# Kernel tuning notes

Hardware: AMD Instinct MI355X
Metric: run time of the kernel (lower is better)

Reference implementation:

```python
import jax, jax.numpy as jnp
import numpy as np

N_CELL = 66
N_SUB = 29934
N = N_CELL + N_SUB  # 30000 nodes
F = 256
E_HALF = 480000
K = 3
LAYERS = 2
BN_EPS = 1e-5


def setup_inputs() -> dict:
    key = jax.random.key(0)
    ks = jax.random.split(key, 8)
    cell_feat = jax.random.normal(ks[0], (N_CELL, F), dtype=jnp.float32)
    sub_feat = jax.random.normal(ks[1], (N_SUB, F), dtype=jnp.float32)
    # interaction_edge builds a symmetric directed edge list: (a,b) and (b,a)
    src = jax.random.randint(ks[2], (E_HALF,), 0, N)
    dst = jax.random.randint(ks[3], (E_HALF,), 0, N)
    edge_index = jnp.stack([jnp.concatenate([src, dst]),
                            jnp.concatenate([dst, src])], axis=0)
    ew_half = jax.random.uniform(ks[4], (E_HALF,), dtype=jnp.float32, minval=0.1, maxval=1.0)
    edge_weight = jnp.concatenate([ew_half, ew_half])
    glorot = np.sqrt(6.0 / (F + F))
    W1 = jax.random.uniform(ks[5], (F, F), dtype=jnp.float32, minval=-glorot, maxval=glorot)
    W2 = jax.random.uniform(ks[6], (F, F), dtype=jnp.float32, minval=-glorot, maxval=glorot)
    b1 = jnp.zeros((F,), jnp.float32)
    b2 = jnp.zeros((F,), jnp.float32)
    prelu_w = jnp.full((F,), 0.25, jnp.float32)  # PReLU default init
    gamma = jnp.ones((F,), jnp.float32)
    beta = jnp.zeros((F,), jnp.float32)
    return {"cell_feat": cell_feat, "sub_feat": sub_feat,
            "edge_index": edge_index, "edge_weight": edge_weight,
            "W1": W1, "b1": b1, "W2": W2, "b2": b2,
            "prelu_w": prelu_w, "gamma": gamma, "beta": beta}


def _gcn_norm(edge_index, edge_weight, n):
    # SGConv's gcn_norm: add self-loops (weight 1), symmetric degree normalization
    loop = jnp.arange(n)
    row = jnp.concatenate([edge_index[0], loop])  # source j
    col = jnp.concatenate([edge_index[1], loop])  # target i
    ew = jnp.concatenate([edge_weight, jnp.ones((n,), edge_weight.dtype)])
    deg = jax.ops.segment_sum(ew, col, num_segments=n)
    dinv = jnp.where(deg > 0, jax.lax.rsqrt(deg), 0.0)
    norm = dinv[row] * ew * dinv[col]
    return row, col, norm


def _sgconv(x, row, col, norm, W, b, n):
    # K-hop propagation: x <- A_hat^K x, then linear
    for _ in range(K):
        x = jax.ops.segment_sum(norm[:, None] * x[row], col, num_segments=n)
    return x @ W.T + b


def _prelu_bn(x, prelu_w, gamma, beta):
    x = jnp.where(x >= 0, x, prelu_w * x)
    mean = jnp.mean(x, axis=0)
    var = jnp.mean(jnp.square(x - mean), axis=0)  # biased, training-mode BN
    return gamma * (x - mean) * jax.lax.rsqrt(var + BN_EPS) + beta


def reference(cell_feat, sub_feat, edge_index, edge_weight,
              W1, b1, W2, b2, prelu_w, gamma, beta):
    x = jnp.concatenate([cell_feat, sub_feat], axis=0)  # [N, F]
    n = x.shape[0]
    row, col, norm = _gcn_norm(edge_index, edge_weight, n)
    for W, b in ((W1, b1), (W2, b2)):
        x = _sgconv(x, row, col, norm, W, b, n)
        x = _prelu_bn(x, prelu_w, gamma, beta)
    return x[:N_CELL, :], x[N_CELL:, :]
```

## Files before the change

### kernel.cpp

```cpp
#include <hip/hip_runtime.h>
#include <hip/hip_bf16.h>

constexpr int NN    = 30000;
constexpr int NCELL = 66;
constexpr int NF    = 256;
constexpr int CAP   = 80;
constexpr float EPS = 1e-5f;

using bf16x8 = __attribute__((ext_vector_type(8))) short;
using f32x4  = __attribute__((ext_vector_type(4))) float;

__device__ __forceinline__ float bf2f(unsigned short u) {
    return __uint_as_float(((unsigned)u) << 16);
}
__device__ __forceinline__ unsigned short f2bf(float f) {
    __hip_bfloat16 h = __float2bfloat16(f);
    return *reinterpret_cast<unsigned short*>(&h);
}
__device__ __forceinline__ void acc8(float* acc, float4 u, float w) {
    unsigned a = __float_as_uint(u.x), b = __float_as_uint(u.y);
    unsigned c = __float_as_uint(u.z), d = __float_as_uint(u.w);
    acc[0] += w * __uint_as_float(a << 16);
    acc[1] += w * __uint_as_float(a & 0xffff0000u);
    acc[2] += w * __uint_as_float(b << 16);
    acc[3] += w * __uint_as_float(b & 0xffff0000u);
    acc[4] += w * __uint_as_float(c << 16);
    acc[5] += w * __uint_as_float(c & 0xffff0000u);
    acc[6] += w * __uint_as_float(d << 16);
    acc[7] += w * __uint_as_float(d & 0xffff0000u);
}

__global__ void k_init(int* fill, float* sums) {
    int i = blockIdx.x * 256 + threadIdx.x;
    if (i < NN) fill[i] = 0;
    if (i < 2 * NF) sums[i] = 0.0f;
}

__global__ void k_zero_stats(float* sums) {
    int i = threadIdx.x;
    if (i < 2 * NF) sums[i] = 0.0f;
}

__global__ void k_cvtw(const float4* __restrict__ W, ushort4* __restrict__ Wh) {
    int idx = blockIdx.x * 256 + threadIdx.x;
    if (idx >= NF * NF / 4) return;
    float4 v = W[idx];
    ushort4 o;
    o.x = f2bf(v.x); o.y = f2bf(v.y); o.z = f2bf(v.z); o.w = f2bf(v.w);
    Wh[idx] = o;
}

__global__ void k_scatter(const int* __restrict__ ei, const float* __restrict__ ew,
                          int* fill, unsigned* __restrict__ bkt, int E) {
    int e = blockIdx.x * 256 + threadIdx.x;
    if (e >= E) return;
    int row = ei[e];
    int col = ei[E + e];
    unsigned q = (unsigned)(ew[e] * 65536.0f);
    int pos = atomicAdd(&fill[col], 1);
    unsigned v = ((unsigned)row) | (q << 16);
    __builtin_nontemporal_store(v, &bkt[(size_t)col * CAP + pos]);
}

__global__ void k_deg(const unsigned* __restrict__ bkt, const int* __restrict__ fill,
                      float* __restrict__ s1, float* __restrict__ s2) {
    int i = blockIdx.x * 256 + threadIdx.x;
    if (i >= NN) return;
    int cnt = fill[i];
    unsigned sq = 0;
    const unsigned* p = bkt + (size_t)i * CAP;
    for (int e = 0; e < cnt; e++) sq += (p[e] >> 16);
    float deg = 1.0f + (float)sq * (1.0f / 65536.0f);
    float di = rsqrtf(deg);
    s2[i] = di;
    s1[i] = di * di;
}

__global__ void k_concat_h(const float4* __restrict__ cell, const float4* __restrict__ sub,
                           const float* __restrict__ dinv, ushort4* __restrict__ xh) {
    int idx = blockIdx.x * 256 + threadIdx.x;
    if (idx >= NN * (NF / 4)) return;
    const int CELL4 = NCELL * (NF / 4);
    float4 v = (idx < CELL4) ? cell[idx] : sub[idx - CELL4];
    float di = dinv[idx >> 6];
    ushort4 o;
    o.x = f2bf(v.x * di); o.y = f2bf(v.y * di);
    o.z = f2bf(v.z * di); o.w = f2bf(v.w * di);
    xh[idx] = o;
}

__global__ __launch_bounds__(256) void k_prop(const ushort* __restrict__ xin,
                                              ushort* __restrict__ xout,
                                              const int* __restrict__ fill,
                                              const unsigned* __restrict__ bkt,
                                              const float* __restrict__ scale) {
    constexpr int NB = NN / 4;
    int c    = blockIdx.x / NB;
    int idx  = blockIdx.x - c * NB;
    int n    = idx * 4 + (threadIdx.x >> 6);
    int lane = threadIdx.x & 63;
    int eg   = lane >> 3;
    int f    = lane & 7;
    const float4* xl = (const float4*)xin + c * 8 + f;
    const unsigned* base = bkt + (size_t)n * CAP;
    int cnt = fill[n];
    float acc[8];
    #pragma unroll
    for (int i = 0; i < 8; i++) acc[i] = 0.f;
    for (int e0 = 0; e0 < cnt; e0 += 32) {
        int e = e0 + eg;
        unsigned m0 = (e < cnt)      ? __builtin_nontemporal_load(base + e)      : 0u;
        unsigned m1 = (e + 8 < cnt)  ? __builtin_nontemporal_load(base + e + 8)  : 0u;
        unsigned m2 = (e + 16 < cnt) ? __builtin_nontemporal_load(base + e + 16) : 0u;
        unsigned m3 = (e + 24 < cnt) ? __builtin_nontemporal_load(base + e + 24) : 0u;
        int r0 = (int)(m0 & 0xffffu), r1 = (int)(m1 & 0xffffu);
        int r2 = (int)(m2 & 0xffffu), r3 = (int)(m3 & 0xffffu);
        float w0 = (float)(m0 >> 16) * (1.0f / 65536.0f);
        float w1 = (float)(m1 >> 16) * (1.0f / 65536.0f);
        float w2 = (float)(m2 >> 16) * (1.0f / 65536.0f);
        float w3 = (float)(m3 >> 16) * (1.0f / 65536.0f);
        float4 u0 = xl[r0 * 32];
        float4 u1 = xl[r1 * 32];
        float4 u2 = xl[r2 * 32];
        float4 u3 = xl[r3 * 32];
        acc8(acc, u0, w0); acc8(acc, u1, w1);
        acc8(acc, u2, w2); acc8(acc, u3, w3);
    }
    #pragma unroll
    for (int i = 0; i < 8; i++) {
        acc[i] += __shfl_xor(acc[i], 8);
        acc[i] += __shfl_xor(acc[i], 16);
        acc[i] += __shfl_xor(acc[i], 32);
    }
    if (eg == 0) {
        float4 u = xl[n * 32];
        acc8(acc, u, 1.0f);
        float sc = scale[n];
        #pragma unroll
        for (int i = 0; i < 8; i++) acc[i] *= sc;
        unsigned p0 = ((unsigned)f2bf(acc[1]) << 16) | f2bf(acc[0]);
        unsigned p1 = ((unsigned)f2bf(acc[3]) << 16) | f2bf(acc[2]);
        unsigned p2 = ((unsigned)f2bf(acc[5]) << 16) | f2bf(acc[4]);
        unsigned p3 = ((unsigned)f2bf(acc[7]) << 16) | f2bf(acc[6]);
        f32x4 o;
        o[0] = __uint_as_float(p0); o[1] = __uint_as_float(p1);
        o[2] = __uint_as_float(p2); o[3] = __uint_as_float(p3);
        __builtin_nontemporal_store(o, (f32x4*)xout + n * 32 + c * 8 + f);
    }
}

__global__ __launch_bounds__(256) void k_gemm_fused(const short* __restrict__ A,
                                                    const short* __restrict__ B,
                                                    const float* __restrict__ bias,
                                                    const float* __restrict__ pw,
                                                    float* __restrict__ y,
                                                    float* __restrict__ sums) {
    constexpr int RT = NN / 16;
    int w    = threadIdx.x >> 6;
    int lane = threadIdx.x & 63;
    int rt   = blockIdx.x * 4 + w;
    int ml   = lane & 15;
    int q    = lane >> 4;
    bool valid = rt < RT;
    __shared__ float red[2][4][NF];
    f32x4 acc[16];
    #pragma unroll
    for (int i = 0; i < 16; i++) acc[i] = (f32x4){0.f, 0.f, 0.f, 0.f};
    if (valid) {
        const short* arow = A + (rt * 16 + ml) * NF + q * 8;
        #pragma unroll
        for (int ks = 0; ks < 8; ks++) {
            bf16x8 a = *(const bf16x8*)(arow + ks * 32);
            #pragma unroll
            for (int nt = 0; nt < 16; nt++) {
                bf16x8 b = *(const bf16x8*)(B + (nt * 16 + ml) * NF + ks * 32 + q * 8);
                acc[nt] = __builtin_amdgcn_mfma_f32_16x16x32_bf16(a, b, acc[nt], 0, 0, 0);
            }
        }
    }
    #pragma unroll
    for (int nt = 0; nt < 16; nt++) {
        int col = nt * 16 + ml;
        float s = 0.f, s2 = 0.f;
        if (valid) {
            float bb = bias[col];
            float pc = pw[col];
            #pragma unroll
            for (int r = 0; r < 4; r++) {
                float v = acc[nt][r] + bb;
                v = (v >= 0.f) ? v : pc * v;
                s += v; s2 += v * v;
                y[(rt * 16 + q * 4 + r) * NF + col] = v;
            }
        }
        s  += __shfl_xor(s, 16);  s  += __shfl_xor(s, 32);
        s2 += __shfl_xor(s2, 16); s2 += __shfl_xor(s2, 32);
        if (lane < 16) { red[0][w][col] = s; red[1][w][col] = s2; }
    }
    __syncthreads();
    int t = threadIdx.x;
    float v0 = red[0][0][t] + red[0][1][t] + red[0][2][t] + red[0][3][t];
    float v1 = red[1][0][t] + red[1][1][t] + red[1][2][t] + red[1][3][t];
    atomicAdd(&sums[t], v0);
    atomicAdd(&sums[NF + t], v1);
}

__global__ void k_finalize(const float* __restrict__ sums, const float* __restrict__ gamma,
                           const float* __restrict__ beta, float* __restrict__ ss) {
    int t = threadIdx.x;
    float mean = sums[t] / (float)NN;
    float var = sums[NF + t] / (float)NN - mean * mean;
    if (var < 0.f) var = 0.f;
    float istd = rsqrtf(var + EPS);
    float sc = gamma[t] * istd;
    ss[t] = sc;
    ss[NF + t] = beta[t] - mean * sc;
}

__global__ void k_apply_h(const float4* __restrict__ y, const float* __restrict__ ss,
                          const float* __restrict__ dinv, ushort4* __restrict__ xh) {
    int idx = blockIdx.x * 256 + threadIdx.x;
    if (idx >= NN * (NF / 4)) return;
    int f = (idx & 63) * 4;
    float di = dinv[idx >> 6];
    float4 v = y[idx];
    ushort4 o;
    o.x = f2bf((v.x * ss[f]     + ss[NF + f])     * di);
    o.y = f2bf((v.y * ss[f + 1] + ss[NF + f + 1]) * di);
    o.z = f2bf((v.z * ss[f + 2] + ss[NF + f + 2]) * di);
    o.w = f2bf((v.w * ss[f + 3] + ss[NF + f + 3]) * di);
    xh[idx] = o;
}

__global__ void k_apply_out(const float4* __restrict__ y, const float* __restrict__ ss,
                            float4* __restrict__ out) {
    int idx = blockIdx.x * 256 + threadIdx.x;
    if (idx >= NN * (NF / 4)) return;
    int f = (idx & 63) * 4;
    float4 v = y[idx];
    float4 o;
    o.x = v.x * ss[f]     + ss[NF + f];
    o.y = v.y * ss[f + 1] + ss[NF + f + 1];
    o.z = v.z * ss[f + 2] + ss[NF + f + 2];
    o.w = v.w * ss[f + 3] + ss[NF + f + 3];
    out[idx] = o;
}

extern "C" void kernel_launch(void* const* d_in, const int* in_sizes, int n_in,
                              void* d_out, int out_size, void* d_ws, size_t ws_size,
                              hipStream_t stream) {
    const float* cell  = (const float*)d_in[0];
    const float* sub   = (const float*)d_in[1];
    const int*   ei    = (const int*)  d_in[2];
    const float* ew    = (const float*)d_in[3];
    const float* W1    = (const float*)d_in[4];
    const float* bias1 = (const float*)d_in[5];
    const float* W2    = (const float*)d_in[6];
    const float* bias2 = (const float*)d_in[7];
    const float* pw    = (const float*)d_in[8];
    const float* gamma = (const float*)d_in[9];
    const float* beta  = (const float*)d_in[10];
    float* out = (float*)d_out;
    const int E = in_sizes[3];

    char* ws = (char*)d_ws;
    size_t off = 0;
    auto alloc = [&](size_t bytes) -> void* {
        void* p = ws + off;
        off = (off + bytes + 255) & ~((size_t)255);
        return p;
    };
    ushort*   xh0  = (ushort*)  alloc((size_t)NN * NF * 2);
    ushort*   xh1  = (ushort*)  alloc((size_t)NN * NF * 2);
    float*    yf   = (float*)   alloc((size_t)NN * NF * 4);
    ushort*   W1h  = (ushort*)  alloc((size_t)NF * NF * 2);
    ushort*   W2h  = (ushort*)  alloc((size_t)NF * NF * 2);
    unsigned* bkt  = (unsigned*)alloc((size_t)NN * CAP * 4);
    int*      fill = (int*)     alloc((size_t)NN * 4);
    float*    s1   = (float*)   alloc((size_t)NN * 4);
    float*    s2   = (float*)   alloc((size_t)NN * 4);
    float*    sums = (float*)   alloc((size_t)2 * NF * 4);
    float*    ss   = (float*)   alloc((size_t)2 * NF * 4);

    const int gN  = (NN + 255) / 256;
    const int gE  = (E + 255) / 256;
    const int gV4 = (NN * NF / 4 + 255) / 256;
    const int gW4 = (NF * NF / 4 + 255) / 256;
    const int gP  = NN;
    const int gG  = (NN / 16 + 3) / 4;

    k_init<<<gN, 256, 0, stream>>>(fill, sums);
    k_cvtw<<<gW4, 256, 0, stream>>>((const float4*)W1, (ushort4*)W1h);
    k_cvtw<<<gW4, 256, 0, stream>>>((const float4*)W2, (ushort4*)W2h);
    k_scatter<<<gE, 256, 0, stream>>>(ei, ew, fill, bkt, E);
    k_deg<<<gN, 256, 0, stream>>>(bkt, fill, s1, s2);
    k_concat_h<<<gV4, 256, 0, stream>>>((const float4*)cell, (const float4*)sub, s2, (ushort4*)xh0);

    k_prop<<<gP, 256, 0, stream>>>(xh0, xh1, fill, bkt, s1);
    k_prop<<<gP, 256, 0, stream>>>(xh1, xh0, fill, bkt, s1);
    k_prop<<<gP, 256, 0, stream>>>(xh0, xh1, fill, bkt, s2);
    k_gemm_fused<<<gG, 256, 0, stream>>>((const short*)xh1, (const short*)W1h, bias1, pw, yf, sums);
    k_finalize<<<1, 256, 0, stream>>>(sums, gamma, beta, ss);
    k_apply_h<<<gV4, 256, 0, stream>>>((const float4*)yf, ss, s2, (ushort4*)xh0);
    k_zero_stats<<<1, 512, 0, stream>>>(sums);

    k_prop<<<gP, 256, 0, stream>>>(xh0, xh1, fill, bkt, s1);
    k_prop<<<gP, 256, 0, stream>>>(xh1, xh0, fill, bkt, s1);
    k_prop<<<gP, 256, 0, stream>>>(xh0, xh1, fill, bkt, s2);
    k_gemm_fused<<<gG, 256, 0, stream>>>((const short*)xh1, (const short*)W2h, bias2, pw, yf, sums);
    k_finalize<<<1, 256, 0, stream>>>(sums, gamma, beta, ss);
    k_apply_out<<<gV4, 256, 0, stream>>>((const float4*)yf, ss, (float4*)out);
}
```

Before: 680.2 us.

## Split propagation into per-feature-chunk launches with packed FMA accumulation

The single propagation kernel, which covered all four 64-feature chunks in one grid, becomes four sequential launches of one chunk each. Only one chunk's gathered working set (30000 rows × 128 B) is live at a time, which is meant to raise L2/MALL hit rates on the random neighbor gathers. The inner loop also drops from four to two edges per iteration, accumulates with packed two-wide float vectors to allow packed FMA, and hoists the self-row load and scale read out of the loop. A third buffer stops the second hop from overwriting xh0 while later chunk launches still read it. The cost is 4x more launches and repeated reads of the edge buckets for every chunk.

```diff
diff --git a/kernel.cpp b/kernel.cpp
--- a/kernel.cpp
+++ b/kernel.cpp
@@ -9,6 +9,7 @@
 
 using bf16x8 = __attribute__((ext_vector_type(8))) short;
 using f32x4  = __attribute__((ext_vector_type(4))) float;
+using f32x2  = __attribute__((ext_vector_type(2))) float;
 
 __device__ __forceinline__ float bf2f(unsigned short u) {
     return __uint_as_float(((unsigned)u) << 16);
@@ -16,6 +17,19 @@
 __device__ __forceinline__ unsigned short f2bf(float f) {
     __hip_bfloat16 h = __float2bfloat16(f);
     return *reinterpret_cast<unsigned short*>(&h);
+}
+__device__ __forceinline__ void acc8v(f32x2* acc, float4 u, float w) {
+    unsigned a = __float_as_uint(u.x), b = __float_as_uint(u.y);
+    unsigned c = __float_as_uint(u.z), d = __float_as_uint(u.w);
+    f32x2 wv; wv[0] = w; wv[1] = w;
+    f32x2 e0; e0[0] = __uint_as_float(a << 16); e0[1] = __uint_as_float(a & 0xffff0000u);
+    f32x2 e1; e1[0] = __uint_as_float(b << 16); e1[1] = __uint_as_float(b & 0xffff0000u);
+    f32x2 e2; e2[0] = __uint_as_float(c << 16); e2[1] = __uint_as_float(c & 0xffff0000u);
+    f32x2 e3; e3[0] = __uint_as_float(d << 16); e3[1] = __uint_as_float(d & 0xffff0000u);
+    acc[0] += wv * e0;
+    acc[1] += wv * e1;
+    acc[2] += wv * e2;
+    acc[3] += wv * e3;
 }
 __device__ __forceinline__ void acc8(float* acc, float4 u, float w) {
     unsigned a = __float_as_uint(u.x), b = __float_as_uint(u.y);
@@ -89,59 +103,53 @@
     xh[idx] = o;
 }
 
-__global__ __launch_bounds__(256) void k_prop(const ushort* __restrict__ xin,
-                                              ushort* __restrict__ xout,
-                                              const int* __restrict__ fill,
-                                              const unsigned* __restrict__ bkt,
-                                              const float* __restrict__ scale) {
-    constexpr int NB = NN / 4;
-    int c    = blockIdx.x / NB;
-    int idx  = blockIdx.x - c * NB;
-    int n    = idx * 4 + (threadIdx.x >> 6);
+__global__ __launch_bounds__(256) void k_prop_c(const ushort* __restrict__ xin,
+                                                ushort* __restrict__ xout,
+                                                const int* __restrict__ fill,
+                                                const unsigned* __restrict__ bkt,
+                                                const float* __restrict__ scale,
+                                                int c) {
+    int n    = blockIdx.x * 4 + (threadIdx.x >> 6);
     int lane = threadIdx.x & 63;
     int eg   = lane >> 3;
     int f    = lane & 7;
     const float4* xl = (const float4*)xin + c * 8 + f;
     const unsigned* base = bkt + (size_t)n * CAP;
     int cnt = fill[n];
-    float acc[8];
-    #pragma unroll
-    for (int i = 0; i < 8; i++) acc[i] = 0.f;
-    for (int e0 = 0; e0 < cnt; e0 += 32) {
+    float4 uself = xl[n * 32];
+    float sc = scale[n];
+    f32x2 acc[4];
+    #pragma unroll
+    for (int i = 0; i < 4; i++) { acc[i][0] = 0.f; acc[i][1] = 0.f; }
+    for (int e0 = 0; e0 < cnt; e0 += 16) {
         int e = e0 + eg;
-        unsigned m0 = (e < cnt)      ? __builtin_nontemporal_load(base + e)      : 0u;
-        unsigned m1 = (e + 8 < cnt)  ? __builtin_nontemporal_load(base + e + 8)  : 0u;
-        unsigned m2 = (e + 16 < cnt) ? __builtin_nontemporal_load(base + e + 16) : 0u;
-        unsigned m3 = (e + 24 < cnt) ? __builtin_nontemporal_load(base + e + 24) : 0u;
+        unsigned m0 = (e < cnt)     ? __builtin_nontemporal_load(base + e)     : 0u;
+        unsigned m1 = (e + 8 < cnt) ? __builtin_nontemporal_load(base + e + 8) : 0u;
         int r0 = (int)(m0 & 0xffffu), r1 = (int)(m1 & 0xffffu);
-        int r2 = (int)(m2 & 0xffffu), r3 = (int)(m3 & 0xffffu);
         float w0 = (float)(m0 >> 16) * (1.0f / 65536.0f);
         float w1 = (float)(m1 >> 16) * (1.0f / 65536.0f);
-        float w2 = (float)(m2 >> 16) * (1.0f / 65536.0f);
-        float w3 = (float)(m3 >> 16) * (1.0f / 65536.0f);
         float4 u0 = xl[r0 * 32];
         float4 u1 = xl[r1 * 32];
-        float4 u2 = xl[r2 * 32];
-        float4 u3 = xl[r3 * 32];
-        acc8(acc, u0, w0); acc8(acc, u1, w1);
-        acc8(acc, u2, w2); acc8(acc, u3, w3);
-    }
+        acc8v(acc, u0, w0);
+        acc8v(acc, u1, w1);
+    }
+    float accs[8];
+    #pragma unroll
+    for (int i = 0; i < 4; i++) { accs[2 * i] = acc[i][0]; accs[2 * i + 1] = acc[i][1]; }
     #pragma unroll
     for (int i = 0; i < 8; i++) {
-        acc[i] += __shfl_xor(acc[i], 8);
-        acc[i] += __shfl_xor(acc[i], 16);
-        acc[i] += __shfl_xor(acc[i], 32);
+        accs[i] += __shfl_xor(accs[i], 8);
+        accs[i] += __shfl_xor(accs[i], 16);
+        accs[i] += __shfl_xor(accs[i], 32);
     }
     if (eg == 0) {
-        float4 u = xl[n * 32];
-        acc8(acc, u, 1.0f);
-        float sc = scale[n];
+        acc8(accs, uself, 1.0f);
         #pragma unroll
-        for (int i = 0; i < 8; i++) acc[i] *= sc;
-        unsigned p0 = ((unsigned)f2bf(acc[1]) << 16) | f2bf(acc[0]);
-        unsigned p1 = ((unsigned)f2bf(acc[3]) << 16) | f2bf(acc[2]);
-        unsigned p2 = ((unsigned)f2bf(acc[5]) << 16) | f2bf(acc[4]);
-        unsigned p3 = ((unsigned)f2bf(acc[7]) << 16) | f2bf(acc[6]);
+        for (int i = 0; i < 8; i++) accs[i] *= sc;
+        unsigned p0 = ((unsigned)f2bf(accs[1]) << 16) | f2bf(accs[0]);
+        unsigned p1 = ((unsigned)f2bf(accs[3]) << 16) | f2bf(accs[2]);
+        unsigned p2 = ((unsigned)f2bf(accs[5]) << 16) | f2bf(accs[4]);
+        unsigned p3 = ((unsigned)f2bf(accs[7]) << 16) | f2bf(accs[6]);
         f32x4 o;
         o[0] = __uint_as_float(p0); o[1] = __uint_as_float(p1);
         o[2] = __uint_as_float(p2); o[3] = __uint_as_float(p3);
@@ -272,6 +280,7 @@
     };
     ushort*   xh0  = (ushort*)  alloc((size_t)NN * NF * 2);
     ushort*   xh1  = (ushort*)  alloc((size_t)NN * NF * 2);
+    ushort*   xht  = (ushort*)  alloc((size_t)NN * NF * 2);
     float*    yf   = (float*)   alloc((size_t)NN * NF * 4);
     ushort*   W1h  = (ushort*)  alloc((size_t)NF * NF * 2);
     ushort*   W2h  = (ushort*)  alloc((size_t)NF * NF * 2);
@@ -286,7 +295,7 @@
     const int gE  = (E + 255) / 256;
     const int gV4 = (NN * NF / 4 + 255) / 256;
     const int gW4 = (NF * NF / 4 + 255) / 256;
-    const int gP  = NN;
+    const int gP  = NN / 4;
     const int gG  = (NN / 16 + 3) / 4;
 
     k_init<<<gN, 256, 0, stream>>>(fill, sums);
@@ -296,17 +305,23 @@
     k_deg<<<gN, 256, 0, stream>>>(bkt, fill, s1, s2);
     k_concat_h<<<gV4, 256, 0, stream>>>((const float4*)cell, (const float4*)sub, s2, (ushort4*)xh0);
 
-    k_prop<<<gP, 256, 0, stream>>>(xh0, xh1, fill, bkt, s1);
-    k_prop<<<gP, 256, 0, stream>>>(xh1, xh0, fill, bkt, s1);
-    k_prop<<<gP, 256, 0, stream>>>(xh0, xh1, fill, bkt, s2);
+    for (int c = 0; c < 4; c++)
+        k_prop_c<<<gP, 256, 0, stream>>>(xh0, xh1, fill, bkt, s1, c);
+    for (int c = 0; c < 4; c++)
+        k_prop_c<<<gP, 256, 0, stream>>>(xh1, xht, fill, bkt, s1, c);
+    for (int c = 0; c < 4; c++)
+        k_prop_c<<<gP, 256, 0, stream>>>(xht, xh1, fill, bkt, s2, c);
     k_gemm_fused<<<gG, 256, 0, stream>>>((const short*)xh1, (const short*)W1h, bias1, pw, yf, sums);
     k_finalize<<<1, 256, 0, stream>>>(sums, gamma, beta, ss);
     k_apply_h<<<gV4, 256, 0, stream>>>((const float4*)yf, ss, s2, (ushort4*)xh0);
     k_zero_stats<<<1, 512, 0, stream>>>(sums);
 
-    k_prop<<<gP, 256, 0, stream>>>(xh0, xh1, fill, bkt, s1);
-    k_prop<<<gP, 256, 0, stream>>>(xh1, xh0, fill, bkt, s1);
-    k_prop<<<gP, 256, 0, stream>>>(xh0, xh1, fill, bkt, s2);
+    for (int c = 0; c < 4; c++)
+        k_prop_c<<<gP, 256, 0, stream>>>(xh0, xh1, fill, bkt, s1, c);
+    for (int c = 0; c < 4; c++)
+        k_prop_c<<<gP, 256, 0, stream>>>(xh1, xht, fill, bkt, s1, c);
+    for (int c = 0; c < 4; c++)
+        k_prop_c<<<gP, 256, 0, stream>>>(xht, xh1, fill, bkt, s2, c);
     k_gemm_fused<<<gG, 256, 0, stream>>>((const short*)xh1, (const short*)W2h, bias2, pw, yf, sums);
     k_finalize<<<1, 256, 0, stream>>>(sums, gamma, beta, ss);
     k_apply_out<<<gV4, 256, 0, stream>>>((const float4*)yf, ss, (float4*)out);
```

After: 766.5 us. +12.7%, slower.
